# Kernel tuning notes

Measured on AMD Instinct MI355X. Metric: run time of the kernel, lower is better.

Reference implementation:

```python
import jax, jax.numpy as jnp
import numpy as np

N = 4096
IN_F = 256
HEADS = 8
OUT_F = 64  # per-head dim
NEG_BIG = -9e15


def setup_inputs() -> dict:
    key = jax.random.key(0)
    k1, k2, k3, k4 = jax.random.split(key, 4)
    x = jax.random.normal(k1, (N, IN_F), dtype=jnp.float32)
    adj = jax.random.randint(k2, (N, N), 0, 2, dtype=jnp.int32)
    # linear weight (no bias): torch Linear(in, heads*out) -> store as [in, heads*out]
    lim_w = float(np.sqrt(6.0 / (IN_F + HEADS * OUT_F)))
    W = jax.random.uniform(k3, (IN_F, HEADS * OUT_F), minval=-lim_w, maxval=lim_w, dtype=jnp.float32)
    # attn param [1, heads, 2*out], xavier_uniform
    lim_a = float(np.sqrt(6.0 / (HEADS + 2 * OUT_F)))
    attn = jax.random.uniform(k4, (1, HEADS, 2 * OUT_F), minval=-lim_a, maxval=lim_a, dtype=jnp.float32)
    return {"x": x, "adj": adj, "W": W, "attn": attn}


def reference(x, adj, W, attn):
    n = x.shape[0]
    H = attn.shape[1]
    D = attn.shape[2] // 2
    h = (x @ W).reshape(n, H, D)                       # [N, H, D]
    a_src = attn[0, :, :D]                             # [H, D]
    a_dst = attn[0, :, D:]                             # [H, D]
    # separable GAT score: e[i, j, h] = a_src.h_i + a_dst.h_j
    s_src = jnp.einsum('nhd,hd->nh', h, a_src)         # [N, H]
    s_dst = jnp.einsum('nhd,hd->nh', h, a_dst)         # [N, H]
    e = s_src[:, None, :] + s_dst[None, :, :]          # [N, N, H]
    e = jnp.where(adj[:, :, None] > 0, e, jnp.float32(NEG_BIG))
    attention = jax.nn.softmax(e, axis=1)              # softmax over neighbor dim j
    h_prime = jnp.einsum('ijh,jhd->ihd', attention, h)  # [N, H, D]
    return h_prime.reshape(n, H * D)
```

## Files before the change

kernel.cpp:

```cpp
#include <hip/hip_runtime.h>
#include <hip/hip_bf16.h>
#include <stdint.h>

typedef __attribute__((ext_vector_type(4))) float  f32x4;
typedef __attribute__((ext_vector_type(8))) short  s16x8;
typedef __attribute__((ext_vector_type(4))) int    i32x4;
typedef __attribute__((ext_vector_type(4))) unsigned int u32x4;

#define NN 4096
#define GT_LD 4096
#define NUM_STRIDE (4096 * 512)

__device__ __forceinline__ unsigned short f2bf(float f) {
  uint32_t u = __builtin_bit_cast(uint32_t, f);
  u += 0x7FFF + ((u >> 16) & 1);
  return (unsigned short)(u >> 16);
}

__device__ __forceinline__ void gload_lds16(const void* g, void* l) {
  __builtin_amdgcn_global_load_lds(
      (const __attribute__((address_space(1))) unsigned int*)g,
      (__attribute__((address_space(3))) unsigned int*)l, 16, 0, 0);
}

__global__ __launch_bounds__(512) void k_small(const float* __restrict__ x,
                                               const float* __restrict__ W,
                                               unsigned short* __restrict__ xb,
                                               unsigned short* __restrict__ wt) {
  int bid = blockIdx.x;
  if (bid < 512) {
    int t = bid * 512 + threadIdx.x;
    f32x4 v = ((const f32x4*)x)[t];
    uint64_t r = (uint64_t)f2bf(v.x) | ((uint64_t)f2bf(v.y) << 16) |
                 ((uint64_t)f2bf(v.z) << 32) | ((uint64_t)f2bf(v.w) << 48);
    ((uint64_t*)xb)[t] = r;
  } else {
    int t = (bid - 512) * 512 + threadIdx.x;
    int c = t >> 8, k = t & 255;
    wt[t] = f2bf(W[k * 512 + c]);
  }
}

__global__ __launch_bounds__(512) void k_fat(const int* __restrict__ adj,
                                             unsigned int* __restrict__ bits,
                                             const unsigned short* __restrict__ xb,
                                             const unsigned short* __restrict__ wt,
                                             const float* __restrict__ attn,
                                             unsigned short* __restrict__ gt) {
  __shared__ unsigned short lx[16 * 256];
  __shared__ unsigned short lw[512 * 64];

  if (blockIdx.x >= 256) {
    int row = blockIdx.x - 256;
    int t = threadIdx.x;
    const i32x4* ap = (const i32x4*)(adj + row * 4096) + 2 * t;
    i32x4 v0 = ap[0], v1 = ap[1];
    unsigned b = (v0.x ? 1u : 0u) | (v0.y ? 2u : 0u) |
                 (v0.z ? 4u : 0u) | (v0.w ? 8u : 0u) |
                 (v1.x ? 16u : 0u) | (v1.y ? 32u : 0u) |
                 (v1.z ? 64u : 0u) | (v1.w ? 128u : 0u);
    ((unsigned char*)bits)[row * 512 + t] = (unsigned char)b;
    return;
  }

  const int tid = threadIdx.x;
  const int lane = tid & 63;
  const int h = tid >> 6;
  const int l15 = lane & 15, lg = lane >> 4;
  const int j0 = blockIdx.x * 16;

  {
    int L = tid * 16;
    int row = L >> 9, b = L & 511;
    int sb = b ^ ((row & 7) << 4);
    gload_lds16((const char*)xb + (j0 + row) * 512 + sb, (char*)lx + L);
  }

  f32x4 acc[4] = {};
  for (int kc = 0; kc < 4; ++kc) {
#pragma unroll
    for (int i = 0; i < 8; ++i) {
      int L = (i * 512 + tid) * 16;
      int c = L >> 7, b = L & 127;
      int sb = b ^ ((c & 7) << 4);
      gload_lds16((const char*)wt + c * 512 + kc * 128 + sb, (char*)lw + L);
    }
    asm volatile("s_waitcnt vmcnt(0)");
    __syncthreads();
#pragma unroll
    for (int kk = 0; kk < 2; ++kk) {
      int kby = kk * 64 + lg * 16;
      s16x8 a = *(const s16x8*)((const char*)lx + l15 * 512 +
                                ((kc * 128 + kby) ^ ((l15 & 7) << 4)));
#pragma unroll
      for (int n = 0; n < 4; ++n) {
        int c = h * 64 + n * 16 + l15;
        s16x8 b = *(const s16x8*)((const char*)lw + c * 128 + (kby ^ ((c & 7) << 4)));
        acc[n] = __builtin_amdgcn_mfma_f32_16x16x32_bf16(a, b, acc[n], 0, 0, 0);
      }
    }
    __syncthreads();
  }

  float adv[4];
#pragma unroll
  for (int n = 0; n < 4; ++n) adv[n] = attn[h * 128 + 64 + n * 16 + l15];
#pragma unroll
  for (int r = 0; r < 4; ++r) {
    float p = acc[0][r] * adv[0] + acc[1][r] * adv[1] +
              acc[2][r] * adv[2] + acc[3][r] * adv[3];
#pragma unroll
    for (int m = 1; m < 16; m <<= 1) p += __shfl_xor(p, m);
    float w = expf(p);
    int node = j0 + lg * 4 + r;
#pragma unroll
    for (int n = 0; n < 4; ++n) {
      int c = h * 64 + n * 16 + l15;
      gt[c * GT_LD + node] = f2bf(acc[n][r] * w);
    }
    if (l15 == 0) gt[(512 + h) * GT_LD + node] = f2bf(w);
  }
}

__global__ __launch_bounds__(256, 3) void k_gemm(const unsigned int* __restrict__ bits,
                                                 const unsigned short* __restrict__ GT,
                                                 float* __restrict__ out,
                                                 float* __restrict__ numx,
                                                 float* __restrict__ den,
                                                 int klen) {
  __shared__ unsigned short lB0[128 * 64];
  __shared__ unsigned short lB1[128 * 64];
  __shared__ unsigned short lB2[128 * 64];
  const int tid = threadIdx.x;
  const int lane = tid & 63, wid = tid >> 6;
  const int wr = wid >> 1, wc = wid & 1;
  const int l15 = lane & 15, lg = lane >> 4;
  const int lg8 = lg * 8;

  int g = blockIdx.x;
  int swz = (g & 7) * 20 + (g >> 3);
  int bx = swz / 5, by = swz % 5;
  const int row0 = bx * 128, c0 = by * 128;

  const int s = blockIdx.y;
  float* num = (s == 0) ? out : (numx + (s - 1) * NUM_STRIDE);
  float* dens = den + s * (4096 * 8);

  const uint64_t* ap[4];
#pragma unroll
  for (int m = 0; m < 4; ++m)
    ap[m] = (const uint64_t*)((const char*)bits +
            (size_t)(row0 + wr * 64 + m * 16 + l15) * 512 + (size_t)s * (klen >> 3));

  const char* Bbase = (const char*)GT + c0 * 8192 + (long)s * klen * 2;

  auto stageB = [&](unsigned short* dst, int kt) {
#pragma unroll
    for (int i = 0; i < 4; ++i) {
      int L = (i * 256 + tid) * 16;
      int rr = L >> 7, b = L & 127;
      int sb = b ^ ((rr & 7) << 4);
      gload_lds16(Bbase + rr * 8192 + kt * 128 + sb, (char*)dst + L);
    }
  };

  f32x4 acc[4][4] = {};
  const int NKT = klen >> 6;

  unsigned short *pR = lB0, *pS = lB1, *pF = lB2;

  stageB(pR, 0);
  uint64_t Wc[4];
#pragma unroll
  for (int m = 0; m < 4; ++m) Wc[m] = ap[m][0];

  for (int kt = 0; kt < NKT; ++kt) {
    uint64_t Wn[4] = {0, 0, 0, 0};
    if (kt < NKT - 1) {
      stageB(pS, kt + 1);
#pragma unroll
      for (int m = 0; m < 4; ++m) Wn[m] = ap[m][kt + 1];
    }

    s16x8 af[2][4];
#pragma unroll
    for (int kk = 0; kk < 2; ++kk)
#pragma unroll
      for (int m = 0; m < 4; ++m) {
        uint32_t part = (uint32_t)(Wc[m] >> (kk * 32));
        uint32_t byte = (part >> lg8) & 0xFFu;
        uint32_t t2 = byte | (byte << 15);
        u32x4 w;
#pragma unroll
        for (int d = 0; d < 4; ++d)
          w[d] = ((t2 >> (2 * d)) & 0x10001u) * 0x3F80u;
        af[kk][m] = __builtin_bit_cast(s16x8, w);
      }
    __builtin_amdgcn_sched_barrier(0);

    if (kt < NKT - 1)
      asm volatile("s_waitcnt vmcnt(8)" ::: "memory");
    else
      asm volatile("s_waitcnt vmcnt(0)" ::: "memory");
    __builtin_amdgcn_s_barrier();

    __builtin_amdgcn_s_setprio(1);
#pragma unroll
    for (int kk = 0; kk < 2; ++kk) {
      int kby = kk * 64 + lg * 16;
      s16x8 b[4];
#pragma unroll
      for (int n = 0; n < 4; ++n) {
        int c = wc * 64 + n * 16 + l15;
        b[n] = *(const s16x8*)((const char*)pR + c * 128 + (kby ^ ((c & 7) << 4)));
      }
#pragma unroll
      for (int m = 0; m < 4; ++m)
#pragma unroll
        for (int n = 0; n < 4; ++n)
          acc[m][n] = __builtin_amdgcn_mfma_f32_16x16x32_bf16(af[kk][m], b[n], acc[m][n], 0, 0, 0);
    }
    __builtin_amdgcn_s_setprio(0);

    unsigned short* t = pR; pR = pS; pS = pF; pF = t;
#pragma unroll
    for (int m = 0; m < 4; ++m) Wc[m] = Wn[m];
  }

#pragma unroll
  for (int mm = 0; mm < 4; ++mm)
#pragma unroll
    for (int n = 0; n < 4; ++n) {
      int c = c0 + wc * 64 + n * 16 + l15;
#pragma unroll
      for (int rr = 0; rr < 4; ++rr) {
        int i = row0 + wr * 64 + mm * 16 + lg * 4 + rr;
        float v = acc[mm][n][rr];
        if (c < 512) num[i * 512 + c] = v;
        else if (c < 520) dens[i * 8 + (c - 512)] = v;
      }
    }
}

__global__ __launch_bounds__(256) void k_final(float* __restrict__ out,
                                               const float* __restrict__ numx,
                                               const float* __restrict__ den,
                                               int S) {
  int t = blockIdx.x * 256 + threadIdx.x;
  int i = t >> 7, h = (t >> 4) & 7;
  f32x4 v = ((const f32x4*)out)[t];
  float d = den[i * 8 + h];
  for (int s = 1; s < S; ++s) {
    f32x4 u = ((const f32x4*)(numx + (s - 1) * NUM_STRIDE))[t];
    v.x += u.x; v.y += u.y; v.z += u.z; v.w += u.w;
    d += den[s * 4096 * 8 + i * 8 + h];
  }
  v.x /= d; v.y /= d; v.z /= d; v.w /= d;
  ((f32x4*)out)[t] = v;
}

extern "C" void kernel_launch(void* const* d_in, const int* in_sizes, int n_in,
                              void* d_out, int out_size, void* d_ws, size_t ws_size,
                              hipStream_t stream) {
  const float* x    = (const float*)d_in[0];
  const int*   adj  = (const int*)d_in[1];
  const float* W    = (const float*)d_in[2];
  const float* attn = (const float*)d_in[3];
  float* out = (float*)d_out;
  char* ws = (char*)d_ws;

  unsigned int*   BITS = (unsigned int*)(ws);
  unsigned short* GTp  = (unsigned short*)(ws + 2097152);
  unsigned short* XB   = (unsigned short*)(ws + 6815744);
  unsigned short* WT   = (unsigned short*)(ws + 8912896);
  float*          DEN  = (float*)(ws + 9175040);
  float*          NUMX = (float*)(ws + 9699328);

  int S = 1;
  if (ws_size >= 9699328ull + 3ull * NUM_STRIDE * 4 + 65536) S = 4;
  else if (ws_size >= 9699328ull + 1ull * NUM_STRIDE * 4 + 65536) S = 2;

  k_small<<<768, 512, 0, stream>>>(x, W, XB, WT);
  k_fat  <<<4352, 512, 0, stream>>>(adj, BITS, XB, WT, attn, GTp);
  dim3 ggrid(160, S);
  k_gemm <<<ggrid, 256, 0, stream>>>(BITS, GTp, out, NUMX, DEN, 4096 / S);
  k_final<<<2048, 256, 0, stream>>>(out, NUMX, DEN, S);
}
```

Baseline: 75.59 us.

## Shrink GEMM column tile to 64 and drop triple-buffered LDS pipeline

The masked aggregation GEMM now uses 128x64 output tiles instead of 128x128, giving 288 blocks per split instead of 160 and cutting the columns wasted on the 520-wide padded output. The triple-buffered asynchronous LDS prefetch, with its explicit vmcnt waits and priority hints, is replaced by a single buffer loaded each iteration and guarded by two __syncthreads. The goal is better occupancy and more parallelism. In exchange, loads are no longer overlapped with MFMA work, and each block re-expands the adjacency bits for half as many columns.

```diff
diff --git a/kernel.cpp b/kernel.cpp
--- a/kernel.cpp
+++ b/kernel.cpp
@@ -122,15 +122,13 @@
   }
 }
 
-__global__ __launch_bounds__(256, 3) void k_gemm(const unsigned int* __restrict__ bits,
-                                                 const unsigned short* __restrict__ GT,
-                                                 float* __restrict__ out,
-                                                 float* __restrict__ numx,
-                                                 float* __restrict__ den,
-                                                 int klen) {
-  __shared__ unsigned short lB0[128 * 64];
-  __shared__ unsigned short lB1[128 * 64];
-  __shared__ unsigned short lB2[128 * 64];
+__global__ __launch_bounds__(256) void k_gemm(const unsigned int* __restrict__ bits,
+                                              const unsigned short* __restrict__ GT,
+                                              float* __restrict__ out,
+                                              float* __restrict__ numx,
+                                              float* __restrict__ den,
+                                              int klen) {
+  __shared__ unsigned short lB[64 * 64];
   const int tid = threadIdx.x;
   const int lane = tid & 63, wid = tid >> 6;
   const int wr = wid >> 1, wc = wid & 1;
@@ -138,9 +136,9 @@
   const int lg8 = lg * 8;
 
   int g = blockIdx.x;
-  int swz = (g & 7) * 20 + (g >> 3);
-  int bx = swz / 5, by = swz % 5;
-  const int row0 = bx * 128, c0 = by * 128;
+  int swz = (g & 7) * 36 + (g >> 3);
+  int bx = swz / 9, by = swz % 9;
+  const int row0 = bx * 128, c0 = by * 64;
 
   const int s = blockIdx.y;
   float* num = (s == 0) ? out : (numx + (s - 1) * NUM_STRIDE);
@@ -154,34 +152,30 @@
 
   const char* Bbase = (const char*)GT + c0 * 8192 + (long)s * klen * 2;
 
-  auto stageB = [&](unsigned short* dst, int kt) {
-#pragma unroll
-    for (int i = 0; i < 4; ++i) {
+  auto stageB = [&](int kt) {
+#pragma unroll
+    for (int i = 0; i < 2; ++i) {
       int L = (i * 256 + tid) * 16;
       int rr = L >> 7, b = L & 127;
       int sb = b ^ ((rr & 7) << 4);
-      gload_lds16(Bbase + rr * 8192 + kt * 128 + sb, (char*)dst + L);
+      gload_lds16(Bbase + rr * 8192 + kt * 128 + sb, (char*)lB + L);
     }
   };
 
-  f32x4 acc[4][4] = {};
+  f32x4 acc[4][2] = {};
   const int NKT = klen >> 6;
 
-  unsigned short *pR = lB0, *pS = lB1, *pF = lB2;
-
-  stageB(pR, 0);
   uint64_t Wc[4];
 #pragma unroll
   for (int m = 0; m < 4; ++m) Wc[m] = ap[m][0];
 
   for (int kt = 0; kt < NKT; ++kt) {
+    stageB(kt);
     uint64_t Wn[4] = {0, 0, 0, 0};
     if (kt < NKT - 1) {
-      stageB(pS, kt + 1);
 #pragma unroll
       for (int m = 0; m < 4; ++m) Wn[m] = ap[m][kt + 1];
     }
-
     s16x8 af[2][4];
 #pragma unroll
     for (int kk = 0; kk < 2; ++kk)
@@ -196,46 +190,37 @@
           w[d] = ((t2 >> (2 * d)) & 0x10001u) * 0x3F80u;
         af[kk][m] = __builtin_bit_cast(s16x8, w);
       }
-    __builtin_amdgcn_sched_barrier(0);
-
-    if (kt < NKT - 1)
-      asm volatile("s_waitcnt vmcnt(8)" ::: "memory");
-    else
-      asm volatile("s_waitcnt vmcnt(0)" ::: "memory");
-    __builtin_amdgcn_s_barrier();
-
-    __builtin_amdgcn_s_setprio(1);
+
+    __syncthreads();
 #pragma unroll
     for (int kk = 0; kk < 2; ++kk) {
       int kby = kk * 64 + lg * 16;
-      s16x8 b[4];
-#pragma unroll
-      for (int n = 0; n < 4; ++n) {
-        int c = wc * 64 + n * 16 + l15;
-        b[n] = *(const s16x8*)((const char*)pR + c * 128 + (kby ^ ((c & 7) << 4)));
+      s16x8 b[2];
+#pragma unroll
+      for (int n = 0; n < 2; ++n) {
+        int c = wc * 32 + n * 16 + l15;
+        b[n] = *(const s16x8*)((const char*)lB + c * 128 + (kby ^ ((c & 7) << 4)));
       }
 #pragma unroll
       for (int m = 0; m < 4; ++m)
 #pragma unroll
-        for (int n = 0; n < 4; ++n)
+        for (int n = 0; n < 2; ++n)
           acc[m][n] = __builtin_amdgcn_mfma_f32_16x16x32_bf16(af[kk][m], b[n], acc[m][n], 0, 0, 0);
     }
-    __builtin_amdgcn_s_setprio(0);
-
-    unsigned short* t = pR; pR = pS; pS = pF; pF = t;
+    __syncthreads();
 #pragma unroll
     for (int m = 0; m < 4; ++m) Wc[m] = Wn[m];
   }
 
 #pragma unroll
-  for (int mm = 0; mm < 4; ++mm)
-#pragma unroll
-    for (int n = 0; n < 4; ++n) {
-      int c = c0 + wc * 64 + n * 16 + l15;
-#pragma unroll
-      for (int rr = 0; rr < 4; ++rr) {
-        int i = row0 + wr * 64 + mm * 16 + lg * 4 + rr;
-        float v = acc[mm][n][rr];
+  for (int m = 0; m < 4; ++m)
+#pragma unroll
+    for (int n = 0; n < 2; ++n) {
+      int c = c0 + wc * 32 + n * 16 + l15;
+#pragma unroll
+      for (int r = 0; r < 4; ++r) {
+        int i = row0 + wr * 64 + m * 16 + lg * 4 + r;
+        float v = acc[m][n][r];
         if (c < 512) num[i * 512 + c] = v;
         else if (c < 520) dens[i * 8 + (c - 512)] = v;
       }
@@ -282,7 +267,7 @@
 
   k_small<<<768, 512, 0, stream>>>(x, W, XB, WT);
   k_fat  <<<4352, 512, 0, stream>>>(adj, BITS, XB, WT, attn, GTp);
-  dim3 ggrid(160, S);
+  dim3 ggrid(288, S);
   k_gemm <<<ggrid, 256, 0, stream>>>(BITS, GTp, out, NUMX, DEN, 4096 / S);
   k_final<<<2048, 256, 0, stream>>>(out, NUMX, DEN, S);
 }
```

Result: slower. 91.34 us (+20.8%).
